# Kernel tuning notes

Measured on AMD Instinct MI355X. Metric: run time of the kernel, lower is better.

## Reference

```python
import jax, jax.numpy as jnp
import numpy as np

DIM = 512
NUM_HEADS = 8
HEAD_DIM = DIM // NUM_HEADS


def setup_inputs() -> dict:
    key = jax.random.key(0)
    ks = jax.random.split(key, 9)
    s = 1.0 / np.sqrt(DIM)
    x = jax.random.normal(ks[0], (2, 4096, DIM), dtype=jnp.float32)
    Wq = jax.random.uniform(ks[1], (DIM, DIM), jnp.float32, -s, s)
    bq = jax.random.uniform(ks[2], (DIM,), jnp.float32, -s, s)
    Wk = jax.random.uniform(ks[3], (DIM, DIM), jnp.float32, -s, s)
    bk = jax.random.uniform(ks[4], (DIM,), jnp.float32, -s, s)
    Wv = jax.random.uniform(ks[5], (DIM, DIM), jnp.float32, -s, s)
    bv = jax.random.uniform(ks[6], (DIM,), jnp.float32, -s, s)
    Wo = jax.random.uniform(ks[7], (DIM, DIM), jnp.float32, -s, s)
    bo = jax.random.uniform(ks[8], (DIM,), jnp.float32, -s, s)
    return {"x": x, "Wq": Wq, "bq": bq, "Wk": Wk, "bk": bk,
            "Wv": Wv, "bv": bv, "Wo": Wo, "bo": bo}


def reference(x, Wq, bq, Wk, bk, Wv, bv, Wo, bo):
    B, S, D = x.shape
    H, Hd = NUM_HEADS, HEAD_DIM
    # Linear layers (torch stores weight as [out,in]; here W is [in,out])
    q = (x @ Wq + bq).reshape(B, S, H, Hd).transpose(0, 2, 1, 3)  # [B,H,S,Hd]
    k = (x @ Wk + bk).reshape(B, S, H, Hd).transpose(0, 2, 1, 3)
    v = (x @ Wv + bv).reshape(B, S, H, Hd).transpose(0, 2, 1, 3)
    # NOTE: original scales by dim**0.5, not head_dim**0.5
    energy = jnp.einsum('bhqd,bhkd->bhqk', q, k) / jnp.sqrt(jnp.float32(D))
    attn = jax.nn.softmax(energy, axis=-1)
    out = jnp.einsum('bhqk,bhkd->bhqd', attn, v)
    out = out.transpose(0, 2, 1, 3).reshape(B, S, D)
    return out @ Wo + bo
```

## Files before the change

### kernel.cpp

```cpp
#include <hip/hip_runtime.h>

typedef unsigned short USH;
typedef short s16x8 __attribute__((ext_vector_type(8)));
typedef float f32x4 __attribute__((ext_vector_type(4)));
typedef float f32x4v __attribute__((ext_vector_type(4)));
typedef unsigned int u32x4 __attribute__((ext_vector_type(4)));
typedef s16x8 s16x8_a __attribute__((may_alias));
typedef f32x4v f32x4v_a __attribute__((may_alias));
typedef u32x4 u32x4_a __attribute__((may_alias));
typedef unsigned long long u64_a __attribute__((may_alias));

#if __has_builtin(__builtin_amdgcn_exp2f)
#define EXP2F(x) __builtin_amdgcn_exp2f(x)
#else
#define EXP2F(x) __builtin_exp2f(x)
#endif

__device__ __forceinline__ USH f2bf(float f) {
  union { float f; unsigned int i; } c; c.f = f;
  unsigned int x = c.i;
  return (USH)((x + 0x7FFFu + ((x >> 16) & 1u)) >> 16);
}
__device__ __forceinline__ unsigned int pk_bf16(float a, float b) {
#if __has_builtin(__builtin_amdgcn_cvt_pk_bf16_f32)
  typedef USH ush2 __attribute__((ext_vector_type(2)));
  union { ush2 v; unsigned int u; } r;
  r.v = __builtin_amdgcn_cvt_pk_bf16_f32(a, b);
  return r.u;
#else
  union { float f; unsigned int i; } ca, cb; ca.f = a; cb.f = b;
  return ((ca.i + 0x8000u) >> 16) | ((cb.i + 0x8000u) & 0xFFFF0000u);
#endif
}

__device__ __forceinline__ f32x4 mfma16(s16x8 a, s16x8 b, f32x4 c) {
  return __builtin_amdgcn_mfma_f32_16x16x32_bf16(a, b, c, 0, 0, 0);
}

#if __has_builtin(__builtin_amdgcn_global_load_lds)
#define HAS_GLD 1
__device__ __forceinline__ void gld_lds16(const USH* g, USH* l) {
  __builtin_amdgcn_global_load_lds(
      static_cast<const unsigned int __attribute__((address_space(1)))*>(
          (const void __attribute__((address_space(1)))*)g),
      static_cast<unsigned int __attribute__((address_space(3)))*>(
          (void __attribute__((address_space(3)))*)l),
      16, 0, 0);
}
#else
#define HAS_GLD 0
__device__ __forceinline__ void gld_lds16(const USH* g, USH* l) {
  *(s16x8_a*)l = *(const s16x8_a*)g;
}
#endif

__global__ void transpose_w(const float* __restrict__ Wq, const float* __restrict__ Wk,
                            const float* __restrict__ Wv, const float* __restrict__ Wo,
                            USH* __restrict__ wsT) {
  __shared__ float tile[32][33];
  const int z = blockIdx.z;
  const float* W = (z == 0) ? Wq : (z == 1) ? Wk : (z == 2) ? Wv : Wo;
  USH* WT = wsT + (size_t)z * 262144;
  const int n0 = blockIdx.x * 32, k0 = blockIdx.y * 32;
  const int tx = threadIdx.x, ty = threadIdx.y;
  #pragma unroll
  for (int i = 0; i < 4; ++i)
    tile[ty + i * 8][tx] = W[(size_t)(k0 + ty + i * 8) * 512 + n0 + tx];
  __syncthreads();
  #pragma unroll
  for (int i = 0; i < 4; ++i)
    WT[(size_t)(n0 + ty + i * 8) * 512 + k0 + tx] = f2bf(tile[tx][ty + i * 8]);
}

__global__ __launch_bounds__(256) void cvt_x(const float* __restrict__ x,
                                             USH* __restrict__ xb) {
  const size_t i = ((size_t)blockIdx.x * 256 + threadIdx.x) * 8;
  const f32x4v a = *(const f32x4v_a*)(x + i);
  const f32x4v b = *(const f32x4v_a*)(x + i + 4);
  u32x4 s;
  s.x = pk_bf16(a.x, a.y); s.y = pk_bf16(a.z, a.w);
  s.z = pk_bf16(b.x, b.y); s.w = pk_bf16(b.z, b.w);
  *(u32x4_a*)(xb + i) = s;
}

template <int MODE>
__global__ __launch_bounds__(256, 3) void gemm_bias(
    const USH* __restrict__ A, const USH* __restrict__ BT0,
    const float* __restrict__ b0, const float* __restrict__ b1,
    const float* __restrict__ b2,
    USH* __restrict__ oQ, USH* __restrict__ oKV, float* __restrict__ oF) {
  __shared__ __align__(16) USH As[128 * 68];
  __shared__ __align__(16) USH Bs[128 * 68];
  const int z = blockIdx.z;
  const USH* BT = BT0 + (size_t)z * 262144;
  const float* bias = (z == 0) ? b0 : ((z == 1) ? b1 : b2);
  USH* outb = (z == 0) ? oQ : (oKV + (size_t)(z - 1) * 4194304);
  const float qs = (MODE == 1 && z == 0) ? 0.06375871528132839f : 1.0f;

  const int t = threadIdx.x;
  const int w = t >> 6, lane = t & 63;
  const int c = lane & 15, g = lane >> 4;
  const int wm = w & 1, wn = w >> 1;
  const int m0 = blockIdx.x * 128, n0 = blockIdx.y * 128;
  const int srow = t >> 1, scol = (t & 1) * 32;

  f32x4 acc[4][4] = {};

  const USH* Ap0 = A + (size_t)(m0 + srow) * 512 + scol;
  const USH* Bp0 = BT + (size_t)(n0 + srow) * 512 + scol;
  s16x8 pa[4], pb[4];
  #pragma unroll
  for (int j = 0; j < 4; ++j) {
    pa[j] = *(const s16x8_a*)(Ap0 + j * 8);
    pb[j] = *(const s16x8_a*)(Bp0 + j * 8);
  }

  for (int kt = 0; kt < 8; ++kt) {
    __syncthreads();
    #pragma unroll
    for (int j = 0; j < 4; ++j) {
      *(s16x8_a*)(As + srow * 68 + scol + j * 8) = pa[j];
      *(s16x8_a*)(Bs + srow * 68 + scol + j * 8) = pb[j];
    }
    const int ktn = (kt < 7) ? kt + 1 : kt;
    #pragma unroll
    for (int j = 0; j < 4; ++j) {
      pa[j] = *(const s16x8_a*)(Ap0 + ktn * 64 + j * 8);
      pb[j] = *(const s16x8_a*)(Bp0 + ktn * 64 + j * 8);
    }
    __syncthreads();
    #pragma unroll
    for (int ks = 0; ks < 2; ++ks) {
      s16x8 af[4], bfr[4];
      #pragma unroll
      for (int i = 0; i < 4; ++i) {
        af[i]  = *(const s16x8_a*)(As + (wm * 64 + i * 16 + c) * 68 + ks * 32 + g * 8);
        bfr[i] = *(const s16x8_a*)(Bs + (wn * 64 + i * 16 + c) * 68 + ks * 32 + g * 8);
      }
      #pragma unroll
      for (int mf = 0; mf < 4; ++mf)
        #pragma unroll
        for (int nf = 0; nf < 4; ++nf)
          acc[mf][nf] = mfma16(af[mf], bfr[nf], acc[mf][nf]);
    }
  }

  #pragma unroll
  for (int nf = 0; nf < 4; ++nf) {
    const int n = n0 + wn * 64 + nf * 16 + c;
    const float bv = bias[n];
    #pragma unroll
    for (int mf = 0; mf < 4; ++mf)
      #pragma unroll
      for (int r = 0; r < 4; ++r) {
        const int m = m0 + wm * 64 + mf * 16 + g * 4 + r;
        const float v = (acc[mf][nf][r] + bv) * qs;
        if (MODE == 0) {
          oF[(size_t)m * 512 + n] = v;
        } else {
          const int bb = m >> 12, s = m & 4095, h = n >> 6, hd = n & 63;
          if (z == 2)
            outb[(((size_t)(bb * 8 + h)) * 64 + hd) * 4096 + s] = f2bf(v);
          else
            outb[(((size_t)(bb * 8 + h)) * 4096 + s) * 64 + hd] = f2bf(v);
        }
      }
  }
}

__global__ __launch_bounds__(256, 2) void attn(const USH* __restrict__ Qbuf,
                                               const USH* __restrict__ kv,
                                               USH* __restrict__ att) {
  __shared__ __align__(16) USH Ks[2 * 4096];
  __shared__ __align__(16) USH Vt[2 * 4096];
  __shared__ __align__(16) USH Ps[4][32 * 76];
  __shared__ float lbuf[4][32];

  const int t = threadIdx.x;
  const int w = t >> 6, lane = t & 63;
  const int c = lane & 15, g = lane >> 4;
  const int bh = blockIdx.y;
  const int bb = bh >> 3, hh = bh & 7;
  const size_t base = (size_t)bh * 262144;
  const USH* Q = Qbuf + base;
  const USH* K = kv + base;
  const USH* V = kv + 4194304 + base;
  const int q0 = blockIdx.x * 128 + w * 32;

  s16x8 qf[2][2];
  #pragma unroll
  for (int colf = 0; colf < 2; ++colf)
    #pragma unroll
    for (int kh = 0; kh < 2; ++kh)
      qf[colf][kh] = *(const s16x8_a*)(Q + (size_t)(q0 + colf * 16 + c) * 64 + kh * 32 + g * 8);

  s16x8 onesf;
  {
    const short one = (short)0x3F80, val = (c == 0) ? one : (short)0;
    #pragma unroll
    for (int j = 0; j < 8; ++j) onesf[j] = val;
  }

  f32x4 o[2][4] = {};
  f32x4 o_l[2] = {};

  const int rK = w * 16 + (lane >> 2);
  const int ccK = (lane & 3) ^ ((lane >> 3) & 3);
  const USH* gK0 = K + (size_t)rK * 64 + ccK * 8;
  const int hdV = w * 16 + (lane >> 3);
  const int ccV = (lane & 7) ^ ((lane >> 3) & 7);
  const USH* gV0 = V + (size_t)hdV * 4096 + ccV * 8;
  const USH* gV1 = V + (size_t)(hdV + 8) * 4096 + ccV * 8;
  USH* lK = Ks + w * 512 + lane * 8;
  USH* lV = Vt + w * 1024 + lane * 8;

  gld_lds16(gK0, lK);
  gld_lds16(gK0 + 32, lK + 2048);
  gld_lds16(gV0, lV);
  gld_lds16(gV1, lV + 512);

  for (int kt = 0; kt < 64; ++kt) {
    const int buf = kt & 1;
    __syncthreads();
    if (kt < 63) {
      const int nb = (buf ^ 1) * 4096;
      const size_t kof = (size_t)(kt + 1) * 4096;
      const size_t vof = (size_t)(kt + 1) * 64;
      gld_lds16(gK0 + kof, lK + nb);
      gld_lds16(gK0 + 32 + kof, lK + nb + 2048);
      gld_lds16(gV0 + vof, lV + nb);
      gld_lds16(gV1 + vof, lV + nb + 512);
    }

    f32x4 st[4][2] = {};
    #pragma unroll
    for (int kh = 0; kh < 2; ++kh) {
      s16x8 ak[4];
      #pragma unroll
      for (int kff = 0; kff < 4; ++kff) {
        const int row = kff * 16 + c;
        const int qsw = (g ^ ((c >> 1) & 3)) * 8;
        ak[kff] = *(const s16x8_a*)(Ks + buf * 4096 + kh * 2048 + row * 32 + qsw);
      }
      #pragma unroll
      for (int kff = 0; kff < 4; ++kff)
        #pragma unroll
        for (int colf = 0; colf < 2; ++colf)
          st[kff][colf] = mfma16(ak[kff], qf[colf][kh], st[kff][colf]);
    }

    #pragma unroll
    for (int colf = 0; colf < 2; ++colf)
      #pragma unroll
      for (int kff = 0; kff < 4; ++kff)
        #pragma unroll
        for (int r = 0; r < 4; ++r)
          st[kff][colf][r] = EXP2F(st[kff][colf][r]);

    #pragma unroll
    for (int colf = 0; colf < 2; ++colf)
      #pragma unroll
      for (int kff = 0; kff < 4; ++kff) {
        const unsigned int lo = pk_bf16(st[kff][colf][0], st[kff][colf][1]);
        const unsigned int hi = pk_bf16(st[kff][colf][2], st[kff][colf][3]);
        const unsigned long long pk64 =
            (unsigned long long)lo | ((unsigned long long)hi << 32);
        *(u64_a*)(&Ps[w][(c + 16 * colf) * 76 + kff * 16 + g * 4]) = pk64;
      }

    #pragma unroll
    for (int kf = 0; kf < 2; ++kf) {
      s16x8 ap[2], bv[4];
      #pragma unroll
      for (int mf = 0; mf < 2; ++mf)
        ap[mf] = *(const s16x8_a*)(&Ps[w][(mf * 16 + c) * 76 + kf * 32 + g * 8]);
      #pragma unroll
      for (int hf = 0; hf < 4; ++hf) {
        const int qv = ((kf * 4 + g) ^ (c & 7)) * 8;
        bv[hf] = *(const s16x8_a*)(Vt + buf * 4096 + (c + 16 * hf) * 64 + qv);
      }
      #pragma unroll
      for (int mf = 0; mf < 2; ++mf) {
        #pragma unroll
        for (int hf = 0; hf < 4; ++hf)
          o[mf][hf] = mfma16(ap[mf], bv[hf], o[mf][hf]);
        o_l[mf] = mfma16(ap[mf], onesf, o_l[mf]);
      }
    }
  }

  if (c == 0) {
    #pragma unroll
    for (int mf = 0; mf < 2; ++mf)
      #pragma unroll
      for (int r = 0; r < 4; ++r)
        lbuf[w][mf * 16 + g * 4 + r] = o_l[mf][r];
  }
  __syncthreads();

  #pragma unroll
  for (int mf = 0; mf < 2; ++mf)
    #pragma unroll
    for (int r = 0; r < 4; ++r) {
      const int ml = mf * 16 + g * 4 + r;
      const float linv = 1.0f / lbuf[w][ml];
      const int qrow = q0 + ml;
      #pragma unroll
      for (int hf = 0; hf < 4; ++hf) {
        const int hd = c + 16 * hf;
        att[((size_t)(bb * 4096 + qrow)) * 512 + hh * 64 + hd] =
            f2bf(o[mf][hf][r] * linv);
      }
    }
}

extern "C" void kernel_launch(void* const* d_in, const int* in_sizes, int n_in,
                              void* d_out, int out_size, void* d_ws, size_t ws_size,
                              hipStream_t stream) {
  (void)in_sizes; (void)n_in; (void)out_size; (void)ws_size;
  const float* x  = (const float*)d_in[0];
  const float* Wq = (const float*)d_in[1];
  const float* bq = (const float*)d_in[2];
  const float* Wk = (const float*)d_in[3];
  const float* bk = (const float*)d_in[4];
  const float* Wv = (const float*)d_in[5];
  const float* bv = (const float*)d_in[6];
  const float* Wo = (const float*)d_in[7];
  const float* bo = (const float*)d_in[8];
  USH* ws  = (USH*)d_ws;
  USH* wT  = ws;
  USH* kv  = ws + 1048576;
  USH* att = ws + 1048576 + 8388608;
  float* outF = (float*)d_out;
  USH* qscratch = (USH*)d_out;
  USH* xb = (USH*)d_out + 4194304;

  transpose_w<<<dim3(16, 16, 4), dim3(32, 8), 0, stream>>>(Wq, Wk, Wv, Wo, wT);
  cvt_x<<<2048, 256, 0, stream>>>(x, xb);
  gemm_bias<1><<<dim3(64, 4, 3), 256, 0, stream>>>(xb, wT, bq, bk, bv,
                                                   qscratch, kv, nullptr);
  attn<<<dim3(32, 16), 256, 0, stream>>>(qscratch, kv, att);
  gemm_bias<0><<<dim3(64, 4, 1), 256, 0, stream>>>(att, wT + 3 * 262144, bo, bo, bo,
                                                   nullptr, nullptr, outF);
}
```

Before: 213.6 us.

## Vectorize GEMM epilogue stores via swapped MFMA operands; split attention into 8 waves

In the projection GEMM, the MFMA operand order is swapped for the Q/K and output cases so each lane holds 4 consecutive output columns. That enables 16-byte float stores and 8-byte packed bf16 stores instead of scalar scatters. The V path packs 4 consecutive sequence positions into one 8-byte store. The attention kernel now uses 512 threads with 8 waves of 16 query rows each instead of 4 waves of 32, halving each thread's K/V tile-load share and register state to raise occupancy, at the cost of more LDS traffic per MFMA.

```diff
diff --git a/kernel.cpp b/kernel.cpp
--- a/kernel.cpp
+++ b/kernel.cpp
@@ -38,7 +38,6 @@
 }
 
 #if __has_builtin(__builtin_amdgcn_global_load_lds)
-#define HAS_GLD 1
 __device__ __forceinline__ void gld_lds16(const USH* g, USH* l) {
   __builtin_amdgcn_global_load_lds(
       static_cast<const unsigned int __attribute__((address_space(1)))*>(
@@ -48,7 +47,6 @@
       16, 0, 0);
 }
 #else
-#define HAS_GLD 0
 __device__ __forceinline__ void gld_lds16(const USH* g, USH* l) {
   *(s16x8_a*)l = *(const s16x8_a*)g;
 }
@@ -96,6 +94,7 @@
   const float* bias = (z == 0) ? b0 : ((z == 1) ? b1 : b2);
   USH* outb = (z == 0) ? oQ : (oKV + (size_t)(z - 1) * 4194304);
   const float qs = (MODE == 1 && z == 0) ? 0.06375871528132839f : 1.0f;
+  const bool swp = (MODE == 0) || (z < 2);
 
   const int t = threadIdx.x;
   const int w = t >> 6, lane = t & 63;
@@ -137,44 +136,80 @@
         af[i]  = *(const s16x8_a*)(As + (wm * 64 + i * 16 + c) * 68 + ks * 32 + g * 8);
         bfr[i] = *(const s16x8_a*)(Bs + (wn * 64 + i * 16 + c) * 68 + ks * 32 + g * 8);
       }
-      #pragma unroll
-      for (int mf = 0; mf < 4; ++mf)
+      if (swp) {
         #pragma unroll
         for (int nf = 0; nf < 4; ++nf)
-          acc[mf][nf] = mfma16(af[mf], bfr[nf], acc[mf][nf]);
-    }
-  }
-
-  #pragma unroll
-  for (int nf = 0; nf < 4; ++nf) {
-    const int n = n0 + wn * 64 + nf * 16 + c;
-    const float bv = bias[n];
-    #pragma unroll
-    for (int mf = 0; mf < 4; ++mf)
-      #pragma unroll
-      for (int r = 0; r < 4; ++r) {
-        const int m = m0 + wm * 64 + mf * 16 + g * 4 + r;
-        const float v = (acc[mf][nf][r] + bv) * qs;
-        if (MODE == 0) {
-          oF[(size_t)m * 512 + n] = v;
-        } else {
-          const int bb = m >> 12, s = m & 4095, h = n >> 6, hd = n & 63;
-          if (z == 2)
-            outb[(((size_t)(bb * 8 + h)) * 64 + hd) * 4096 + s] = f2bf(v);
-          else
-            outb[(((size_t)(bb * 8 + h)) * 4096 + s) * 64 + hd] = f2bf(v);
-        }
-      }
-  }
-}
-
-__global__ __launch_bounds__(256, 2) void attn(const USH* __restrict__ Qbuf,
+          #pragma unroll
+          for (int mf = 0; mf < 4; ++mf)
+            acc[nf][mf] = mfma16(bfr[nf], af[mf], acc[nf][mf]);
+      } else {
+        #pragma unroll
+        for (int mf = 0; mf < 4; ++mf)
+          #pragma unroll
+          for (int nf = 0; nf < 4; ++nf)
+            acc[mf][nf] = mfma16(af[mf], bfr[nf], acc[mf][nf]);
+      }
+    }
+  }
+
+  if (MODE == 0) {
+    #pragma unroll
+    for (int nf = 0; nf < 4; ++nf) {
+      const int nb = n0 + wn * 64 + nf * 16 + g * 4;
+      const f32x4v bv4 = *(const f32x4v_a*)(bias + nb);
+      #pragma unroll
+      for (int mf = 0; mf < 4; ++mf) {
+        const int m = m0 + wm * 64 + mf * 16 + c;
+        f32x4v v;
+        #pragma unroll
+        for (int r = 0; r < 4; ++r) v[r] = acc[nf][mf][r] + bv4[r];
+        *(f32x4v_a*)(oF + (size_t)m * 512 + nb) = v;
+      }
+    }
+  } else if (z < 2) {
+    #pragma unroll
+    for (int nf = 0; nf < 4; ++nf) {
+      const int nb = n0 + wn * 64 + nf * 16 + g * 4;
+      const int h = nb >> 6, hd0 = nb & 63;
+      const f32x4v bv4 = *(const f32x4v_a*)(bias + nb);
+      #pragma unroll
+      for (int mf = 0; mf < 4; ++mf) {
+        const int m = m0 + wm * 64 + mf * 16 + c;
+        const int bb = m >> 12, s = m & 4095;
+        const unsigned int lo = pk_bf16((acc[nf][mf][0] + bv4[0]) * qs,
+                                        (acc[nf][mf][1] + bv4[1]) * qs);
+        const unsigned int hi = pk_bf16((acc[nf][mf][2] + bv4[2]) * qs,
+                                        (acc[nf][mf][3] + bv4[3]) * qs);
+        *(u64_a*)(outb + ((size_t)(bb * 8 + h) * 4096 + s) * 64 + hd0) =
+            (unsigned long long)lo | ((unsigned long long)hi << 32);
+      }
+    }
+  } else {
+    #pragma unroll
+    for (int nf = 0; nf < 4; ++nf) {
+      const int n = n0 + wn * 64 + nf * 16 + c;
+      const int h = n >> 6, hd = n & 63;
+      const float bv = bias[n];
+      #pragma unroll
+      for (int mf = 0; mf < 4; ++mf) {
+        const int mb = m0 + wm * 64 + mf * 16 + g * 4;
+        const int bb = mb >> 12, s0 = mb & 4095;
+        const unsigned int lo = pk_bf16(acc[mf][nf][0] + bv, acc[mf][nf][1] + bv);
+        const unsigned int hi = pk_bf16(acc[mf][nf][2] + bv, acc[mf][nf][3] + bv);
+        *(u64_a*)(outb + ((size_t)(bb * 8 + h) * 64 + hd) * 4096 + s0) =
+            (unsigned long long)lo | ((unsigned long long)hi << 32);
+      }
+    }
+  }
+}
+
+__global__ __launch_bounds__(512, 4) void attn(const USH* __restrict__ Qbuf,
                                                const USH* __restrict__ kv,
                                                USH* __restrict__ att) {
   __shared__ __align__(16) USH Ks[2 * 4096];
   __shared__ __align__(16) USH Vt[2 * 4096];
-  __shared__ __align__(16) USH Ps[4][32 * 76];
-  __shared__ float lbuf[4][32];
+  __shared__ __align__(16) USH Ps[8][16 * 76];
+  __shared__ float lbuf[8][16];
 
   const int t = threadIdx.x;
   const int w = t >> 6, lane = t & 63;
@@ -185,14 +220,12 @@
   const USH* Q = Qbuf + base;
   const USH* K = kv + base;
   const USH* V = kv + 4194304 + base;
-  const int q0 = blockIdx.x * 128 + w * 32;
-
-  s16x8 qf[2][2];
-  #pragma unroll
-  for (int colf = 0; colf < 2; ++colf)
-    #pragma unroll
-    for (int kh = 0; kh < 2; ++kh)
-      qf[colf][kh] = *(const s16x8_a*)(Q + (size_t)(q0 + colf * 16 + c) * 64 + kh * 32 + g * 8);
+  const int q0 = blockIdx.x * 128 + w * 16;
+
+  s16x8 qf[2];
+  #pragma unroll
+  for (int kh = 0; kh < 2; ++kh)
+    qf[kh] = *(const s16x8_a*)(Q + (size_t)(q0 + c) * 64 + kh * 32 + g * 8);
 
   s16x8 onesf;
   {
@@ -201,38 +234,32 @@
     for (int j = 0; j < 8; ++j) onesf[j] = val;
   }
 
-  f32x4 o[2][4] = {};
-  f32x4 o_l[2] = {};
-
-  const int rK = w * 16 + (lane >> 2);
-  const int ccK = (lane & 3) ^ ((lane >> 3) & 3);
-  const USH* gK0 = K + (size_t)rK * 64 + ccK * 8;
-  const int hdV = w * 16 + (lane >> 3);
-  const int ccV = (lane & 7) ^ ((lane >> 3) & 7);
+  f32x4 o[4] = {};
+  f32x4 o_l = {};
+
+  const int pK = w * 16 + (lane >> 2);
+  const int keyK = pK & 63, halfK = pK >> 6;
+  const int ccK = (lane & 3) ^ ((keyK >> 1) & 3);
+  const USH* gK0 = K + (size_t)keyK * 64 + halfK * 32 + ccK * 8;
+  const int hdV = w * 8 + (lane >> 3);
+  const int ccV = (lane & 7) ^ (hdV & 7);
   const USH* gV0 = V + (size_t)hdV * 4096 + ccV * 8;
-  const USH* gV1 = V + (size_t)(hdV + 8) * 4096 + ccV * 8;
   USH* lK = Ks + w * 512 + lane * 8;
-  USH* lV = Vt + w * 1024 + lane * 8;
+  USH* lV = Vt + w * 512 + lane * 8;
 
   gld_lds16(gK0, lK);
-  gld_lds16(gK0 + 32, lK + 2048);
   gld_lds16(gV0, lV);
-  gld_lds16(gV1, lV + 512);
 
   for (int kt = 0; kt < 64; ++kt) {
     const int buf = kt & 1;
     __syncthreads();
     if (kt < 63) {
       const int nb = (buf ^ 1) * 4096;
-      const size_t kof = (size_t)(kt + 1) * 4096;
-      const size_t vof = (size_t)(kt + 1) * 64;
-      gld_lds16(gK0 + kof, lK + nb);
-      gld_lds16(gK0 + 32 + kof, lK + nb + 2048);
-      gld_lds16(gV0 + vof, lV + nb);
-      gld_lds16(gV1 + vof, lV + nb + 512);
-    }
-
-    f32x4 st[4][2] = {};
+      gld_lds16(gK0 + (size_t)(kt + 1) * 4096, lK + nb);
+      gld_lds16(gV0 + (size_t)(kt + 1) * 64, lV + nb);
+    }
+
+    f32x4 st[4] = {};
     #pragma unroll
     for (int kh = 0; kh < 2; ++kh) {
       s16x8 ak[4];
@@ -244,74 +271,57 @@
       }
       #pragma unroll
       for (int kff = 0; kff < 4; ++kff)
-        #pragma unroll
-        for (int colf = 0; colf < 2; ++colf)
-          st[kff][colf] = mfma16(ak[kff], qf[colf][kh], st[kff][colf]);
-    }
-
-    #pragma unroll
-    for (int colf = 0; colf < 2; ++colf)
-      #pragma unroll
-      for (int kff = 0; kff < 4; ++kff)
-        #pragma unroll
-        for (int r = 0; r < 4; ++r)
-          st[kff][colf][r] = EXP2F(st[kff][colf][r]);
-
-    #pragma unroll
-    for (int colf = 0; colf < 2; ++colf)
-      #pragma unroll
-      for (int kff = 0; kff < 4; ++kff) {
-        const unsigned int lo = pk_bf16(st[kff][colf][0], st[kff][colf][1]);
-        const unsigned int hi = pk_bf16(st[kff][colf][2], st[kff][colf][3]);
-        const unsigned long long pk64 =
-            (unsigned long long)lo | ((unsigned long long)hi << 32);
-        *(u64_a*)(&Ps[w][(c + 16 * colf) * 76 + kff * 16 + g * 4]) = pk64;
-      }
+        st[kff] = mfma16(ak[kff], qf[kh], st[kff]);
+    }
+
+    #pragma unroll
+    for (int kff = 0; kff < 4; ++kff)
+      #pragma unroll
+      for (int r = 0; r < 4; ++r)
+        st[kff][r] = EXP2F(st[kff][r]);
+
+    #pragma unroll
+    for (int kff = 0; kff < 4; ++kff) {
+      const unsigned int lo = pk_bf16(st[kff][0], st[kff][1]);
+      const unsigned int hi = pk_bf16(st[kff][2], st[kff][3]);
+      *(u64_a*)(&Ps[w][c * 76 + kff * 16 + g * 4]) =
+          (unsigned long long)lo | ((unsigned long long)hi << 32);
+    }
 
     #pragma unroll
     for (int kf = 0; kf < 2; ++kf) {
-      s16x8 ap[2], bv[4];
-      #pragma unroll
-      for (int mf = 0; mf < 2; ++mf)
-        ap[mf] = *(const s16x8_a*)(&Ps[w][(mf * 16 + c) * 76 + kf * 32 + g * 8]);
+      const s16x8 ap = *(const s16x8_a*)(&Ps[w][c * 76 + kf * 32 + g * 8]);
+      s16x8 bv[4];
       #pragma unroll
       for (int hf = 0; hf < 4; ++hf) {
         const int qv = ((kf * 4 + g) ^ (c & 7)) * 8;
         bv[hf] = *(const s16x8_a*)(Vt + buf * 4096 + (c + 16 * hf) * 64 + qv);
       }
       #pragma unroll
-      for (int mf = 0; mf < 2; ++mf) {
-        #pragma unroll
-        for (int hf = 0; hf < 4; ++hf)
-          o[mf][hf] = mfma16(ap[mf], bv[hf], o[mf][hf]);
-        o_l[mf] = mfma16(ap[mf], onesf, o_l[mf]);
-      }
+      for (int hf = 0; hf < 4; ++hf)
+        o[hf] = mfma16(ap, bv[hf], o[hf]);
+      o_l = mfma16(ap, onesf, o_l);
     }
   }
 
   if (c == 0) {
     #pragma unroll
-    for (int mf = 0; mf < 2; ++mf)
-      #pragma unroll
-      for (int r = 0; r < 4; ++r)
-        lbuf[w][mf * 16 + g * 4 + r] = o_l[mf][r];
+    for (int r = 0; r < 4; ++r) lbuf[w][g * 4 + r] = o_l[r];
   }
   __syncthreads();
 
   #pragma unroll
-  for (int mf = 0; mf < 2; ++mf)
-    #pragma unroll
-    for (int r = 0; r < 4; ++r) {
-      const int ml = mf * 16 + g * 4 + r;
-      const float linv = 1.0f / lbuf[w][ml];
-      const int qrow = q0 + ml;
-      #pragma unroll
-      for (int hf = 0; hf < 4; ++hf) {
-        const int hd = c + 16 * hf;
-        att[((size_t)(bb * 4096 + qrow)) * 512 + hh * 64 + hd] =
-            f2bf(o[mf][hf][r] * linv);
-      }
-    }
+  for (int r = 0; r < 4; ++r) {
+    const int ml = g * 4 + r;
+    const float linv = 1.0f / lbuf[w][ml];
+    const int qrow = q0 + ml;
+    #pragma unroll
+    for (int hf = 0; hf < 4; ++hf) {
+      const int hd = c + 16 * hf;
+      att[((size_t)(bb * 4096 + qrow)) * 512 + hh * 64 + hd] =
+          f2bf(o[hf][r] * linv);
+    }
+  }
 }
 
 extern "C" void kernel_launch(void* const* d_in, const int* in_sizes, int n_in,
@@ -339,7 +349,7 @@
   cvt_x<<<2048, 256, 0, stream>>>(x, xb);
   gemm_bias<1><<<dim3(64, 4, 3), 256, 0, stream>>>(xb, wT, bq, bk, bv,
                                                    qscratch, kv, nullptr);
-  attn<<<dim3(32, 16), 256, 0, stream>>>(qscratch, kv, att);
+  attn<<<dim3(32, 16), 512, 0, stream>>>(qscratch, kv, att);
   gemm_bias<0><<<dim3(64, 4, 1), 256, 0, stream>>>(att, wT + 3 * 262144, bo, bo, bo,
                                                    nullptr, nullptr, outF);
 }
```

New measurement: 253.4 us. +18.6%, slower.
